# Optimization experiments

Measured on AMD Instinct MI355X. Metric: run time of the kernel, lower is better.

## Reference

```python
import jax, jax.numpy as jnp
import numpy as np

TEMPERATURE = 8.0  # sqrt(head_dim=64)
NEG_INF = -1e9


def setup_inputs() -> dict:
    key = jax.random.key(0)
    kq, kk, kv, km = jax.random.split(key, 4)
    B, H, S, D = 4, 16, 2048, 64
    q = jax.random.normal(kq, (B, H, S, D), dtype=jnp.float32)
    k = jax.random.normal(kk, (B, H, S, D), dtype=jnp.float32)
    v = jax.random.normal(kv, (B, H, S, D), dtype=jnp.float32)
    mask = jax.random.randint(km, (B, 1, S, S), 0, 2).astype(jnp.int32)
    return {"q": q, "k": k, "v": v, "mask": mask}


def reference(q, k, v, mask):
    # attn = (q / T) @ k^T  -> [B,H,S,S]
    attn = jnp.einsum('bhqd,bhkd->bhqk', q / TEMPERATURE, k)
    # masked_fill(mask == 0, -1e9)
    attn = jnp.where(mask == 0, NEG_INF, attn)
    # softmax over keys (dropout omitted: eval mode / deterministic baseline)
    attn = jax.nn.softmax(attn, axis=-1)
    out = jnp.einsum('bhqk,bhkd->bhqd', attn, v)
    return (out, attn)
```

## Files before the change

kernel.cpp:

```cpp
#include <hip/hip_runtime.h>
#include <stdint.h>

#define S_LEN 2048
#define DHEAD 64
#define BATCH 4
#define HEADS 16
#define QBLK 32
#define KBLK 64
#define NT 32
#define NBLK 4096
#define NEG_BIG (-1e9f)

typedef _Float16 half4v __attribute__((ext_vector_type(4)));
typedef _Float16 half8v __attribute__((ext_vector_type(8)));
typedef float floatx4 __attribute__((ext_vector_type(4)));

#define QH_OFF 0u
#define KH_OFF 16777216u
#define VT_OFF 33554432u
#define BM_OFF 50331648u

#define WAITV(N) asm volatile("s_waitcnt vmcnt(" #N ")" ::: "memory")
#define WAITL()  asm volatile("s_waitcnt lgkmcnt(0)" ::: "memory")
#define FENCE()  asm volatile("" ::: "memory")
#define BAR()    __builtin_amdgcn_s_barrier()

__device__ __forceinline__ void glds16(const void* g, void* l) {
    __builtin_amdgcn_global_load_lds(
        (const __attribute__((address_space(1))) uint32_t*)g,
        (__attribute__((address_space(3))) uint32_t*)(uint32_t)(uintptr_t)l,
        16, 0, 0);
}

__global__ __launch_bounds__(256) void prep_qk(const float* __restrict__ q, const float* __restrict__ k,
                                               _Float16* __restrict__ qh, _Float16* __restrict__ kh) {
    int i = blockIdx.x * 256 + threadIdx.x;
    const float* src; _Float16* dst; float s;
    if (i < 1048576) { src = q + (size_t)i * 8; dst = qh + (size_t)i * 8; s = 0.125f; }
    else { int j = i - 1048576; src = k + (size_t)j * 8; dst = kh + (size_t)j * 8; s = 1.0f; }
    floatx4 a = *(const floatx4*)src;
    floatx4 b = *(const floatx4*)(src + 4);
    half8v h;
    h[0]=(_Float16)(a[0]*s); h[1]=(_Float16)(a[1]*s); h[2]=(_Float16)(a[2]*s); h[3]=(_Float16)(a[3]*s);
    h[4]=(_Float16)(b[0]*s); h[5]=(_Float16)(b[1]*s); h[6]=(_Float16)(b[2]*s); h[7]=(_Float16)(b[3]*s);
    *(half8v*)dst = h;
}

__global__ __launch_bounds__(256) void prep_vt(const float* __restrict__ v, _Float16* __restrict__ vt) {
    __shared__ _Float16 lt[64][72];
    int bh = blockIdx.x >> 5;
    int s0 = (blockIdx.x & 31) * 64;
    int t  = threadIdx.x;
    {
        int row = t >> 2, dq = t & 3;
        const float* vb = v + ((size_t)bh * S_LEN + s0 + row) * DHEAD + dq * 16;
        #pragma unroll
        for (int q = 0; q < 4; ++q) {
            floatx4 val = *(const floatx4*)(vb + q * 4);
            #pragma unroll
            for (int j = 0; j < 4; ++j) lt[dq * 16 + q * 4 + j][row] = (_Float16)val[j];
        }
    }
    __syncthreads();
    {
        int d = t >> 2, kq = t & 3;
        half8v h0 = *(const half8v*)&lt[d][kq * 16];
        half8v h1 = *(const half8v*)&lt[d][kq * 16 + 8];
        _Float16* dst = vt + (size_t)bh * DHEAD * S_LEN + (size_t)d * S_LEN + s0 + kq * 16;
        *(half8v*)dst = h0;
        *(half8v*)(dst + 8) = h1;
    }
}

__global__ __launch_bounds__(256) void prep_bm(const int* __restrict__ mask, unsigned long long* __restrict__ bm) {
    int lane = threadIdx.x & 63, w = threadIdx.x >> 6;
    size_t row = (size_t)blockIdx.x * 4 + w;
    const int* mrow = mask + row * S_LEN;
    unsigned long long* brow = bm + row * 32;
    #pragma unroll 4
    for (int t = 0; t < 32; ++t) {
        unsigned long long bits = __ballot(mrow[t * 64 + lane] != 0);
        if (lane == 0) brow[t] = bits;
    }
}

__global__ __launch_bounds__(512, 8)
void attn_main(const _Float16* __restrict__ qh, const _Float16* __restrict__ kh,
               const _Float16* __restrict__ vt, const uint32_t* __restrict__ bm,
               float* __restrict__ outg, float* __restrict__ attng)
{
    __shared__ _Float16 kb[2][KBLK * DHEAD];
    __shared__ _Float16 vb[2][KBLK * DHEAD];
    __shared__ _Float16 pb[QBLK * KBLK];
    __shared__ float zb[4][QBLK];

    const int tid  = threadIdx.x;
    const int lane = tid & 63;
    const int w    = tid >> 6;
    const int c    = lane & 15;
    const int g    = lane >> 4;
    const int rh   = w >> 2;
    const int kgrp = w & 3;

    const int raw = blockIdx.x;
    const int lb  = (raw & 7) * (NBLK / 8) + (raw >> 3);
    const int bh  = lb >> 6;
    const int q0  = (lb & 63) * QBLK;
    const int bb  = bh >> 4;

    const _Float16* qp = qh + (size_t)bh * S_LEN * DHEAD;
    const char* kpc = (const char*)(kh + (size_t)bh * S_LEN * DHEAD);
    const char* vpc = (const char*)(vt + (size_t)bh * DHEAD * S_LEN);
    float* outp  = outg  + (size_t)bh * S_LEN * DHEAD;
    float* attnp = attng + (size_t)bh * S_LEN * S_LEN;

    const int srow = w * 8 + (lane >> 3);
    const int sq   = (lane & 7) ^ (srow & 7);
    const char* ksrc = kpc + srow * 128 + sq * 16;
    const char* vsrc = vpc + srow * (S_LEN * 2) + sq * 16;

    half8v qf0, qf1;
    {
        const _Float16* qb = qp + (q0 + rh * 16 + c) * DHEAD + g * 8;
        qf0 = *(const half8v*)qb;
        qf1 = *(const half8v*)(qb + 32);
    }

    const int keyl  = kgrp * 16 + c;
    const int koff0 = keyl * 128 + ((g ^ (c & 7)) << 4);
    const int koff1 = keyl * 128 + (((4 + g) ^ (c & 7)) << 4);
    const int prow  = rh * 16 + c;
    const int poff0 = prow * 128 + ((g ^ (c & 7)) << 4);
    const int poff1 = prow * 128 + (((4 + g) ^ (c & 7)) << 4);

    const int bmbit = (kgrp & 1) * 16 + c;
    const uint32_t* bmb = bm + ((size_t)bb * S_LEN + q0 + rh * 16 + g * 4) * (NT * 2) + (kgrp >> 1);

    int pwo0, pwo1, pwo2, pwo3;
    {
        int q8 = keyl >> 3, b2 = (keyl & 7) << 1;
        int r0 = rh * 16 + g * 4;
        pwo0 = (((r0 + 0) * 8 + (q8 ^ ((r0 + 0) & 7))) << 4) + b2;
        pwo1 = (((r0 + 1) * 8 + (q8 ^ ((r0 + 1) & 7))) << 4) + b2;
        pwo2 = (((r0 + 2) * 8 + (q8 ^ ((r0 + 2) & 7))) << 4) + b2;
        pwo3 = (((r0 + 3) * 8 + (q8 ^ ((r0 + 3) & 7))) << 4) + b2;
    }

    const int arow = tid >> 4, aq = tid & 15;
    const int aroff = ((arow * 8 + ((aq >> 1) ^ (arow & 7))) << 4) + ((aq & 1) << 3);
    float* abase = attnp + (size_t)(q0 + arow) * S_LEN + aq * 4;

    uint32_t bc0, bc1, bc2, bc3, bn0, bn1, bn2, bn3;

    float z0 = 0.f, z1 = 0.f, z2 = 0.f, z3 = 0.f;
    glds16(ksrc, (char*)&kb[0][0] + w * 1024);
    bc0 = bmb[0]; bc1 = bmb[64]; bc2 = bmb[128]; bc3 = bmb[192];
    #pragma unroll 1
    for (int t = 0; t < NT; ++t) {
        BAR(); FENCE();
        if (t + 1 < NT) {
            glds16(ksrc + (t + 1) * 8192, (char*)&kb[(t + 1) & 1][0] + w * 1024);
            int i2 = (t + 1) * 2;
            bn0 = bmb[i2]; bn1 = bmb[64 + i2]; bn2 = bmb[128 + i2]; bn3 = bmb[192 + i2];
            WAITV(5);
        } else { WAITV(0); }
        BAR(); FENCE();
        const char* kbB = (const char*)&kb[t & 1][0];
        half8v b0 = *(const half8v*)(kbB + koff0);
        half8v b1 = *(const half8v*)(kbB + koff1);
        floatx4 acc = {0.f, 0.f, 0.f, 0.f};
        acc = __builtin_amdgcn_mfma_f32_16x16x32_f16(qf0, b0, acc, 0, 0, 0);
        acc = __builtin_amdgcn_mfma_f32_16x16x32_f16(qf1, b1, acc, 0, 0, 0);
        z0 += __expf(((bc0 >> bmbit) & 1u) ? acc[0] : NEG_BIG);
        z1 += __expf(((bc1 >> bmbit) & 1u) ? acc[1] : NEG_BIG);
        z2 += __expf(((bc2 >> bmbit) & 1u) ? acc[2] : NEG_BIG);
        z3 += __expf(((bc3 >> bmbit) & 1u) ? acc[3] : NEG_BIG);
        bc0 = bn0; bc1 = bn1; bc2 = bn2; bc3 = bn3;
    }
    #pragma unroll
    for (int off = 1; off <= 8; off <<= 1) {
        z0 += __shfl_xor(z0, off); z1 += __shfl_xor(z1, off);
        z2 += __shfl_xor(z2, off); z3 += __shfl_xor(z3, off);
    }
    if (c == 0) {
        int r0 = rh * 16 + g * 4;
        zb[kgrp][r0] = z0; zb[kgrp][r0 + 1] = z1; zb[kgrp][r0 + 2] = z2; zb[kgrp][r0 + 3] = z3;
    }
    WAITL(); BAR(); FENCE();
    float r0_, r1_, r2_, r3_;
    {
        int r0 = rh * 16 + g * 4;
        r0_ = 1.f / (zb[0][r0] + zb[1][r0] + zb[2][r0] + zb[3][r0]);
        r1_ = 1.f / (zb[0][r0+1] + zb[1][r0+1] + zb[2][r0+1] + zb[3][r0+1]);
        r2_ = 1.f / (zb[0][r0+2] + zb[1][r0+2] + zb[2][r0+2] + zb[3][r0+2]);
        r3_ = 1.f / (zb[0][r0+3] + zb[1][r0+3] + zb[2][r0+3] + zb[3][r0+3]);
    }

    floatx4 o = {0.f, 0.f, 0.f, 0.f};
    glds16(ksrc, (char*)&kb[0][0] + w * 1024);
    glds16(vsrc, (char*)&vb[0][0] + w * 1024);
    bc0 = bmb[0]; bc1 = bmb[64]; bc2 = bmb[128]; bc3 = bmb[192];
    #pragma unroll 1
    for (int t = 0; t < NT; ++t) {
        BAR(); FENCE();
        if (t + 1 < NT) {
            glds16(ksrc + (t + 1) * 8192, (char*)&kb[(t + 1) & 1][0] + w * 1024);
            glds16(vsrc + (t + 1) * 128,  (char*)&vb[(t + 1) & 1][0] + w * 1024);
            int i2 = (t + 1) * 2;
            bn0 = bmb[i2]; bn1 = bmb[64 + i2]; bn2 = bmb[128 + i2]; bn3 = bmb[192 + i2];
            if (t == 0) { WAITV(6); } else { WAITV(7); }
        } else { WAITV(1); }
        BAR(); FENCE();
        const char* kbB = (const char*)&kb[t & 1][0];
        half8v b0 = *(const half8v*)(kbB + koff0);
        half8v b1 = *(const half8v*)(kbB + koff1);
        floatx4 acc = {0.f, 0.f, 0.f, 0.f};
        acc = __builtin_amdgcn_mfma_f32_16x16x32_f16(qf0, b0, acc, 0, 0, 0);
        acc = __builtin_amdgcn_mfma_f32_16x16x32_f16(qf1, b1, acc, 0, 0, 0);
        float p0 = __expf(((bc0 >> bmbit) & 1u) ? acc[0] : NEG_BIG) * r0_;
        float p1 = __expf(((bc1 >> bmbit) & 1u) ? acc[1] : NEG_BIG) * r1_;
        float p2 = __expf(((bc2 >> bmbit) & 1u) ? acc[2] : NEG_BIG) * r2_;
        float p3 = __expf(((bc3 >> bmbit) & 1u) ? acc[3] : NEG_BIG) * r3_;
        bc0 = bn0; bc1 = bn1; bc2 = bn2; bc3 = bn3;
        char* pbB = (char*)&pb[0];
        *(_Float16*)(pbB + pwo0) = (_Float16)p0;
        *(_Float16*)(pbB + pwo1) = (_Float16)p1;
        *(_Float16*)(pbB + pwo2) = (_Float16)p2;
        *(_Float16*)(pbB + pwo3) = (_Float16)p3;
        WAITL(); BAR(); FENCE();
        {
            half4v pv4 = *(const half4v*)((const char*)&pb[0] + aroff);
            floatx4 st = {(float)pv4[0], (float)pv4[1], (float)pv4[2], (float)pv4[3]};
            __builtin_nontemporal_store(st, (floatx4*)(abase + t * KBLK));
        }
        const char* vbB = (const char*)&vb[t & 1][0];
        half8v a0 = *(const half8v*)((const char*)&pb[0] + poff0);
        half8v a1 = *(const half8v*)((const char*)&pb[0] + poff1);
        half8v v0 = *(const half8v*)(vbB + koff0);
        half8v v1 = *(const half8v*)(vbB + koff1);
        o = __builtin_amdgcn_mfma_f32_16x16x32_f16(a0, v0, o, 0, 0, 0);
        o = __builtin_amdgcn_mfma_f32_16x16x32_f16(a1, v1, o, 0, 0, 0);
    }
    {
        float* ob = outp + (size_t)(q0 + rh * 16 + g * 4) * DHEAD + kgrp * 16 + c;
        ob[0] = o[0]; ob[DHEAD] = o[1]; ob[2 * DHEAD] = o[2]; ob[3 * DHEAD] = o[3];
    }
}

extern "C" void kernel_launch(void* const* d_in, const int* in_sizes, int n_in,
                              void* d_out, int out_size, void* d_ws, size_t ws_size,
                              hipStream_t stream) {
    const float* q    = (const float*)d_in[0];
    const float* k    = (const float*)d_in[1];
    const float* v    = (const float*)d_in[2];
    const int*   mask = (const int*)d_in[3];
    float* out  = (float*)d_out;
    float* attn = out + (size_t)BATCH * HEADS * S_LEN * DHEAD;

    char* ws = (char*)d_ws;
    _Float16* qhw = (_Float16*)(ws + QH_OFF);
    _Float16* khw = (_Float16*)(ws + KH_OFF);
    _Float16* vtw = (_Float16*)(ws + VT_OFF);
    unsigned long long* bmw = (unsigned long long*)(ws + BM_OFF);

    prep_qk<<<dim3(8192), dim3(256), 0, stream>>>(q, k, qhw, khw);
    prep_vt<<<dim3(2048), dim3(256), 0, stream>>>(v, vtw);
    prep_bm<<<dim3(2048), dim3(256), 0, stream>>>(mask, bmw);
    attn_main<<<dim3(NBLK), dim3(512), 0, stream>>>(qhw, khw, vtw, (const uint32_t*)bmw, out, attn);
}
```

Measured before the change: 376.7 us.

## Transpose QK^T MFMA to keep P in registers and split-K reduce PV

Measured after the change: 604.7 us. +60.5%, slower.

```diff
diff --git a/kernel.cpp b/kernel.cpp
--- a/kernel.cpp
+++ b/kernel.cpp
@@ -89,18 +89,18 @@
                const _Float16* __restrict__ vt, const uint32_t* __restrict__ bm,
                float* __restrict__ outg, float* __restrict__ attng)
 {
-    __shared__ _Float16 kb[2][KBLK * DHEAD];
-    __shared__ _Float16 vb[2][KBLK * DHEAD];
-    __shared__ _Float16 pb[QBLK * KBLK];
-    __shared__ float zb[4][QBLK];
+    __shared__ __attribute__((aligned(16))) char smem[33280];
+    char* kbuf = smem;
+    char* vbuf = smem + 16384;
+    float* zb  = (float*)(smem + 32768);
 
     const int tid  = threadIdx.x;
     const int lane = tid & 63;
     const int w    = tid >> 6;
     const int c    = lane & 15;
     const int g    = lane >> 4;
+    const int kg   = w & 3;
     const int rh   = w >> 2;
-    const int kgrp = w & 3;
 
     const int raw = blockIdx.x;
     const int lb  = (raw & 7) * (NBLK / 8) + (raw >> 3);
@@ -118,6 +118,8 @@
     const int sq   = (lane & 7) ^ (srow & 7);
     const char* ksrc = kpc + srow * 128 + sq * 16;
     const char* vsrc = vpc + srow * (S_LEN * 2) + sq * 16;
+    char* kdst = kbuf + w * 1024;
+    char* vdst = vbuf + w * 1024;
 
     half8v qf0, qf1;
     {
@@ -125,125 +127,109 @@
         qf0 = *(const half8v*)qb;
         qf1 = *(const half8v*)(qb + 32);
     }
-
-    const int keyl  = kgrp * 16 + c;
-    const int koff0 = keyl * 128 + ((g ^ (c & 7)) << 4);
-    const int koff1 = keyl * 128 + (((4 + g) ^ (c & 7)) << 4);
-    const int prow  = rh * 16 + c;
-    const int poff0 = prow * 128 + ((g ^ (c & 7)) << 4);
-    const int poff1 = prow * 128 + (((4 + g) ^ (c & 7)) << 4);
-
-    const int bmbit = (kgrp & 1) * 16 + c;
-    const uint32_t* bmb = bm + ((size_t)bb * S_LEN + q0 + rh * 16 + g * 4) * (NT * 2) + (kgrp >> 1);
-
-    int pwo0, pwo1, pwo2, pwo3;
-    {
-        int q8 = keyl >> 3, b2 = (keyl & 7) << 1;
-        int r0 = rh * 16 + g * 4;
-        pwo0 = (((r0 + 0) * 8 + (q8 ^ ((r0 + 0) & 7))) << 4) + b2;
-        pwo1 = (((r0 + 1) * 8 + (q8 ^ ((r0 + 1) & 7))) << 4) + b2;
-        pwo2 = (((r0 + 2) * 8 + (q8 ^ ((r0 + 2) & 7))) << 4) + b2;
-        pwo3 = (((r0 + 3) * 8 + (q8 ^ ((r0 + 3) & 7))) << 4) + b2;
-    }
-
-    const int arow = tid >> 4, aq = tid & 15;
-    const int aroff = ((arow * 8 + ((aq >> 1) ^ (arow & 7))) << 4) + ((aq & 1) << 3);
-    float* abase = attnp + (size_t)(q0 + arow) * S_LEN + aq * 4;
-
-    uint32_t bc0, bc1, bc2, bc3, bn0, bn1, bn2, bn3;
-
-    float z0 = 0.f, z1 = 0.f, z2 = 0.f, z3 = 0.f;
-    glds16(ksrc, (char*)&kb[0][0] + w * 1024);
-    bc0 = bmb[0]; bc1 = bmb[64]; bc2 = bmb[128]; bc3 = bmb[192];
+    const int koff0 = (kg * 16 + c) * 128 + ((g ^ (c & 7)) << 4);
+    const int koff1 = (kg * 16 + c) * 128 + (((4 + g) ^ (c & 7)) << 4);
+    const int voffb = c * 128 + ((((kg * 2) + (g >> 1)) ^ (c & 7)) << 4) + ((g & 1) << 3);
+    const int bmsh = (kg & 1) * 16 + g * 4;
+    const uint32_t* bmb = bm + ((size_t)bb * S_LEN + q0 + rh * 16 + c) * 64 + (kg >> 1);
+
+    float z = 0.f;
+    glds16(ksrc, kdst);
+    FENCE();
+    uint32_t bc = bmb[0], bn = 0;
     #pragma unroll 1
     for (int t = 0; t < NT; ++t) {
+        FENCE();
+        WAITV(1);
         BAR(); FENCE();
         if (t + 1 < NT) {
-            glds16(ksrc + (t + 1) * 8192, (char*)&kb[(t + 1) & 1][0] + w * 1024);
-            int i2 = (t + 1) * 2;
-            bn0 = bmb[i2]; bn1 = bmb[64 + i2]; bn2 = bmb[128 + i2]; bn3 = bmb[192 + i2];
-            WAITV(5);
-        } else { WAITV(0); }
-        BAR(); FENCE();
-        const char* kbB = (const char*)&kb[t & 1][0];
-        half8v b0 = *(const half8v*)(kbB + koff0);
-        half8v b1 = *(const half8v*)(kbB + koff1);
+            glds16(ksrc + (t + 1) * 8192, kdst + (((t + 1) & 1) << 13));
+            FENCE();
+            bn = bmb[(t + 1) * 2];
+        }
+        const char* kbB = kbuf + ((t & 1) << 13);
+        half8v kf0 = *(const half8v*)(kbB + koff0);
+        half8v kf1 = *(const half8v*)(kbB + koff1);
         floatx4 acc = {0.f, 0.f, 0.f, 0.f};
-        acc = __builtin_amdgcn_mfma_f32_16x16x32_f16(qf0, b0, acc, 0, 0, 0);
-        acc = __builtin_amdgcn_mfma_f32_16x16x32_f16(qf1, b1, acc, 0, 0, 0);
-        z0 += __expf(((bc0 >> bmbit) & 1u) ? acc[0] : NEG_BIG);
-        z1 += __expf(((bc1 >> bmbit) & 1u) ? acc[1] : NEG_BIG);
-        z2 += __expf(((bc2 >> bmbit) & 1u) ? acc[2] : NEG_BIG);
-        z3 += __expf(((bc3 >> bmbit) & 1u) ? acc[3] : NEG_BIG);
-        bc0 = bn0; bc1 = bn1; bc2 = bn2; bc3 = bn3;
-    }
-    #pragma unroll
-    for (int off = 1; off <= 8; off <<= 1) {
-        z0 += __shfl_xor(z0, off); z1 += __shfl_xor(z1, off);
-        z2 += __shfl_xor(z2, off); z3 += __shfl_xor(z3, off);
-    }
-    if (c == 0) {
-        int r0 = rh * 16 + g * 4;
-        zb[kgrp][r0] = z0; zb[kgrp][r0 + 1] = z1; zb[kgrp][r0 + 2] = z2; zb[kgrp][r0 + 3] = z3;
-    }
+        acc = __builtin_amdgcn_mfma_f32_16x16x32_f16(kf0, qf0, acc, 0, 0, 0);
+        acc = __builtin_amdgcn_mfma_f32_16x16x32_f16(kf1, qf1, acc, 0, 0, 0);
+        unsigned bits = bc >> bmsh;
+        z += __expf((bits & 1u) ? acc[0] : NEG_BIG) + __expf((bits & 2u) ? acc[1] : NEG_BIG)
+           + __expf((bits & 4u) ? acc[2] : NEG_BIG) + __expf((bits & 8u) ? acc[3] : NEG_BIG);
+        bc = bn;
+    }
+    z += __shfl_xor(z, 16);
+    z += __shfl_xor(z, 32);
+    if (g == 0) zb[kg * 32 + rh * 16 + c] = z;
     WAITL(); BAR(); FENCE();
-    float r0_, r1_, r2_, r3_;
-    {
-        int r0 = rh * 16 + g * 4;
-        r0_ = 1.f / (zb[0][r0] + zb[1][r0] + zb[2][r0] + zb[3][r0]);
-        r1_ = 1.f / (zb[0][r0+1] + zb[1][r0+1] + zb[2][r0+1] + zb[3][r0+1]);
-        r2_ = 1.f / (zb[0][r0+2] + zb[1][r0+2] + zb[2][r0+2] + zb[3][r0+2]);
-        r3_ = 1.f / (zb[0][r0+3] + zb[1][r0+3] + zb[2][r0+3] + zb[3][r0+3]);
-    }
-
-    floatx4 o = {0.f, 0.f, 0.f, 0.f};
-    glds16(ksrc, (char*)&kb[0][0] + w * 1024);
-    glds16(vsrc, (char*)&vb[0][0] + w * 1024);
-    bc0 = bmb[0]; bc1 = bmb[64]; bc2 = bmb[128]; bc3 = bmb[192];
+    const int row = rh * 16 + c;
+    const float r = 1.0f / (zb[row] + zb[32 + row] + zb[64 + row] + zb[96 + row]);
+
+    floatx4 o0 = {0.f,0.f,0.f,0.f}, o1 = o0, o2 = o0, o3 = o0;
+    float* abase = attnp + (size_t)(q0 + rh * 16 + c) * S_LEN + kg * 16 + g * 4;
+    glds16(ksrc, kdst);
+    glds16(vsrc, vdst);
+    FENCE();
+    bc = bmb[0];
     #pragma unroll 1
     for (int t = 0; t < NT; ++t) {
+        FENCE();
+        if (t == 0) { WAITV(1); } else { WAITV(2); }
         BAR(); FENCE();
         if (t + 1 < NT) {
-            glds16(ksrc + (t + 1) * 8192, (char*)&kb[(t + 1) & 1][0] + w * 1024);
-            glds16(vsrc + (t + 1) * 128,  (char*)&vb[(t + 1) & 1][0] + w * 1024);
-            int i2 = (t + 1) * 2;
-            bn0 = bmb[i2]; bn1 = bmb[64 + i2]; bn2 = bmb[128 + i2]; bn3 = bmb[192 + i2];
-            if (t == 0) { WAITV(6); } else { WAITV(7); }
-        } else { WAITV(1); }
-        BAR(); FENCE();
-        const char* kbB = (const char*)&kb[t & 1][0];
-        half8v b0 = *(const half8v*)(kbB + koff0);
-        half8v b1 = *(const half8v*)(kbB + koff1);
+            glds16(ksrc + (t + 1) * 8192, kdst + (((t + 1) & 1) << 13));
+            glds16(vsrc + (t + 1) * 128,  vdst + (((t + 1) & 1) << 13));
+            FENCE();
+            bn = bmb[(t + 1) * 2];
+        }
+        const char* kbB = kbuf + ((t & 1) << 13);
+        const char* vbB = vbuf + ((t & 1) << 13);
+        half8v kf0 = *(const half8v*)(kbB + koff0);
+        half8v kf1 = *(const half8v*)(kbB + koff1);
         floatx4 acc = {0.f, 0.f, 0.f, 0.f};
-        acc = __builtin_amdgcn_mfma_f32_16x16x32_f16(qf0, b0, acc, 0, 0, 0);
-        acc = __builtin_amdgcn_mfma_f32_16x16x32_f16(qf1, b1, acc, 0, 0, 0);
-        float p0 = __expf(((bc0 >> bmbit) & 1u) ? acc[0] : NEG_BIG) * r0_;
-        float p1 = __expf(((bc1 >> bmbit) & 1u) ? acc[1] : NEG_BIG) * r1_;
-        float p2 = __expf(((bc2 >> bmbit) & 1u) ? acc[2] : NEG_BIG) * r2_;
-        float p3 = __expf(((bc3 >> bmbit) & 1u) ? acc[3] : NEG_BIG) * r3_;
-        bc0 = bn0; bc1 = bn1; bc2 = bn2; bc3 = bn3;
-        char* pbB = (char*)&pb[0];
-        *(_Float16*)(pbB + pwo0) = (_Float16)p0;
-        *(_Float16*)(pbB + pwo1) = (_Float16)p1;
-        *(_Float16*)(pbB + pwo2) = (_Float16)p2;
-        *(_Float16*)(pbB + pwo3) = (_Float16)p3;
-        WAITL(); BAR(); FENCE();
-        {
-            half4v pv4 = *(const half4v*)((const char*)&pb[0] + aroff);
-            floatx4 st = {(float)pv4[0], (float)pv4[1], (float)pv4[2], (float)pv4[3]};
-            __builtin_nontemporal_store(st, (floatx4*)(abase + t * KBLK));
-        }
-        const char* vbB = (const char*)&vb[t & 1][0];
-        half8v a0 = *(const half8v*)((const char*)&pb[0] + poff0);
-        half8v a1 = *(const half8v*)((const char*)&pb[0] + poff1);
-        half8v v0 = *(const half8v*)(vbB + koff0);
-        half8v v1 = *(const half8v*)(vbB + koff1);
-        o = __builtin_amdgcn_mfma_f32_16x16x32_f16(a0, v0, o, 0, 0, 0);
-        o = __builtin_amdgcn_mfma_f32_16x16x32_f16(a1, v1, o, 0, 0, 0);
-    }
-    {
-        float* ob = outp + (size_t)(q0 + rh * 16 + g * 4) * DHEAD + kgrp * 16 + c;
-        ob[0] = o[0]; ob[DHEAD] = o[1]; ob[2 * DHEAD] = o[2]; ob[3 * DHEAD] = o[3];
+        acc = __builtin_amdgcn_mfma_f32_16x16x32_f16(kf0, qf0, acc, 0, 0, 0);
+        acc = __builtin_amdgcn_mfma_f32_16x16x32_f16(kf1, qf1, acc, 0, 0, 0);
+        unsigned bits = bc >> bmsh;
+        float p0 = __expf((bits & 1u) ? acc[0] : NEG_BIG) * r;
+        float p1 = __expf((bits & 2u) ? acc[1] : NEG_BIG) * r;
+        float p2 = __expf((bits & 4u) ? acc[2] : NEG_BIG) * r;
+        float p3 = __expf((bits & 8u) ? acc[3] : NEG_BIG) * r;
+        bc = bn;
+        floatx4 st = {p0, p1, p2, p3};
+        *(floatx4*)(abase + t * KBLK) = st;
+        half4v af; af[0] = (_Float16)p0; af[1] = (_Float16)p1;
+        af[2] = (_Float16)p2; af[3] = (_Float16)p3;
+        half4v bv0 = *(const half4v*)(vbB + voffb);
+        half4v bv1 = *(const half4v*)(vbB + voffb + 2048);
+        half4v bv2 = *(const half4v*)(vbB + voffb + 4096);
+        half4v bv3 = *(const half4v*)(vbB + voffb + 6144);
+        o0 = __builtin_amdgcn_mfma_f32_16x16x16f16(af, bv0, o0, 0, 0, 0);
+        o1 = __builtin_amdgcn_mfma_f32_16x16x16f16(af, bv1, o1, 0, 0, 0);
+        o2 = __builtin_amdgcn_mfma_f32_16x16x16f16(af, bv2, o2, 0, 0, 0);
+        o3 = __builtin_amdgcn_mfma_f32_16x16x16f16(af, bv3, o3, 0, 0, 0);
+    }
+
+    FENCE(); WAITL(); BAR(); FENCE();
+    floatx4* rbuf = (floatx4*)smem;
+    if (kg != 0) {
+        floatx4* rb = rbuf + ((kg - 1) * 2 + rh) * 256 + lane;
+        rb[0] = o0; rb[64] = o1; rb[128] = o2; rb[192] = o3;
+    }
+    WAITL(); BAR(); FENCE();
+    if (kg == 0) {
+        const int s0 = rh * 256 + lane;
+        o0 += rbuf[s0]       + rbuf[512 + s0]       + rbuf[1024 + s0];
+        o1 += rbuf[s0 + 64]  + rbuf[512 + s0 + 64]  + rbuf[1024 + s0 + 64];
+        o2 += rbuf[s0 + 128] + rbuf[512 + s0 + 128] + rbuf[1024 + s0 + 128];
+        o3 += rbuf[s0 + 192] + rbuf[512 + s0 + 192] + rbuf[1024 + s0 + 192];
+        float* ob = outp + (size_t)(q0 + rh * 16 + g * 4) * DHEAD + c;
+        #pragma unroll
+        for (int i = 0; i < 4; ++i) {
+            ob[i * DHEAD]      = o0[i];
+            ob[i * DHEAD + 16] = o1[i];
+            ob[i * DHEAD + 32] = o2[i];
+            ob[i * DHEAD + 48] = o3[i];
+        }
     }
 }
 
```

## Make first softmax pass barrier-free with per-wave private K buffers

Applied to the files above, without the earlier changes.

Result: no change. 380.9 us (+1.1%).

```diff
diff --git a/kernel.cpp b/kernel.cpp
--- a/kernel.cpp
+++ b/kernel.cpp
@@ -89,18 +89,19 @@
                const _Float16* __restrict__ vt, const uint32_t* __restrict__ bm,
                float* __restrict__ outg, float* __restrict__ attng)
 {
-    __shared__ _Float16 kb[2][KBLK * DHEAD];
-    __shared__ _Float16 vb[2][KBLK * DHEAD];
-    __shared__ _Float16 pb[QBLK * KBLK];
-    __shared__ float zb[4][QBLK];
+    __shared__ __attribute__((aligned(16))) char smem[37376];
+    char* kbuf = smem;
+    char* vbuf = smem + 16384;
+    char* pb   = smem + 32768;
+    float* zbf = (float*)(smem + 36864);
 
     const int tid  = threadIdx.x;
     const int lane = tid & 63;
     const int w    = tid >> 6;
     const int c    = lane & 15;
     const int g    = lane >> 4;
+    const int kg   = w & 3;
     const int rh   = w >> 2;
-    const int kgrp = w & 3;
 
     const int raw = blockIdx.x;
     const int lb  = (raw & 7) * (NBLK / 8) + (raw >> 3);
@@ -114,10 +115,12 @@
     float* outp  = outg  + (size_t)bh * S_LEN * DHEAD;
     float* attnp = attng + (size_t)bh * S_LEN * S_LEN;
 
-    const int srow = w * 8 + (lane >> 3);
+    const int srow = tid >> 3;
     const int sq   = (lane & 7) ^ (srow & 7);
     const char* ksrc = kpc + srow * 128 + sq * 16;
     const char* vsrc = vpc + srow * (S_LEN * 2) + sq * 16;
+    char* kdst = kbuf + w * 1024;
+    char* vdst = vbuf + w * 1024;
 
     half8v qf0, qf1;
     {
@@ -125,19 +128,20 @@
         qf0 = *(const half8v*)qb;
         qf1 = *(const half8v*)(qb + 32);
     }
-
-    const int keyl  = kgrp * 16 + c;
-    const int koff0 = keyl * 128 + ((g ^ (c & 7)) << 4);
-    const int koff1 = keyl * 128 + (((4 + g) ^ (c & 7)) << 4);
+    const int koff0 = (kg * 16 + c) * 128 + ((g ^ (c & 7)) << 4);
+    const int koff1 = (kg * 16 + c) * 128 + (((4 + g) ^ (c & 7)) << 4);
     const int prow  = rh * 16 + c;
     const int poff0 = prow * 128 + ((g ^ (c & 7)) << 4);
     const int poff1 = prow * 128 + (((4 + g) ^ (c & 7)) << 4);
-
-    const int bmbit = (kgrp & 1) * 16 + c;
-    const uint32_t* bmb = bm + ((size_t)bb * S_LEN + q0 + rh * 16 + g * 4) * (NT * 2) + (kgrp >> 1);
+    const int koff0p = c * 128 + ((g ^ (c & 7)) << 4);
+    const int koff1p = c * 128 + (((4 + g) ^ (c & 7)) << 4);
+
+    const int bmbit = (kg & 1) * 16 + c;
+    const uint32_t* bmb = bm + ((size_t)bb * S_LEN + q0 + rh * 16 + g * 4) * 64 + (kg >> 1);
 
     int pwo0, pwo1, pwo2, pwo3;
     {
+        int keyl = kg * 16 + c;
         int q8 = keyl >> 3, b2 = (keyl & 7) << 1;
         int r0 = rh * 16 + g * 4;
         pwo0 = (((r0 + 0) * 8 + (q8 ^ ((r0 + 0) & 7))) << 4) + b2;
@@ -145,73 +149,90 @@
         pwo2 = (((r0 + 2) * 8 + (q8 ^ ((r0 + 2) & 7))) << 4) + b2;
         pwo3 = (((r0 + 3) * 8 + (q8 ^ ((r0 + 3) & 7))) << 4) + b2;
     }
-
-    const int arow = tid >> 4, aq = tid & 15;
-    const int aroff = ((arow * 8 + ((aq >> 1) ^ (arow & 7))) << 4) + ((aq & 1) << 3);
-    float* abase = attnp + (size_t)(q0 + arow) * S_LEN + aq * 4;
-
-    uint32_t bc0, bc1, bc2, bc3, bn0, bn1, bn2, bn3;
+    const int ar = tid >> 4, aq = tid & 15;
+    const int proff = ar * 128 + (((aq >> 1) ^ (ar & 7)) << 4) + ((aq & 1) << 3);
+    float* abase = attnp + (size_t)(q0 + ar) * S_LEN + aq * 4;
 
     float z0 = 0.f, z1 = 0.f, z2 = 0.f, z3 = 0.f;
-    glds16(ksrc, (char*)&kb[0][0] + w * 1024);
+    char* myb = smem + w * 4096;
+    const char* kps = kpc + kg * 2048 + (lane >> 3) * 128
+                    + (((lane & 7) ^ ((lane >> 3) & 7)) << 4);
+    glds16(kps, myb);
+    glds16(kps + 1024, myb + 1024);
+    FENCE();
+    uint32_t bc0 = bmb[0], bc1 = bmb[64], bc2 = bmb[128], bc3 = bmb[192];
+    FENCE();
+    glds16(kps + 8192, myb + 2048);
+    glds16(kps + 9216, myb + 3072);
+    FENCE();
+    uint32_t bn0 = 0, bn1 = 0, bn2 = 0, bn3 = 0;
+    #pragma unroll 1
+    for (int t = 0; t < NT; ++t) {
+        FENCE();
+        if (t == NT - 1) { WAITV(0); } else { WAITV(2); }
+        char* kbB = myb + ((t & 1) << 11);
+        half8v kf0 = *(const half8v*)(kbB + koff0p);
+        half8v kf1 = *(const half8v*)(kbB + koff1p);
+        WAITL(); FENCE();
+        if (t + 1 < NT) {
+            int i2 = (t + 1) * 2;
+            bn0 = bmb[i2]; bn1 = bmb[64 + i2]; bn2 = bmb[128 + i2]; bn3 = bmb[192 + i2];
+            FENCE();
+        }
+        if (t + 2 < NT) {
+            const char* s = kps + (t + 2) * 8192;
+            glds16(s, kbB);
+            glds16(s + 1024, kbB + 1024);
+            FENCE();
+        }
+        floatx4 acc = {0.f, 0.f, 0.f, 0.f};
+        acc = __builtin_amdgcn_mfma_f32_16x16x32_f16(qf0, kf0, acc, 0, 0, 0);
+        acc = __builtin_amdgcn_mfma_f32_16x16x32_f16(qf1, kf1, acc, 0, 0, 0);
+        z0 += __expf(((bc0 >> bmbit) & 1u) ? acc[0] : NEG_BIG);
+        z1 += __expf(((bc1 >> bmbit) & 1u) ? acc[1] : NEG_BIG);
+        z2 += __expf(((bc2 >> bmbit) & 1u) ? acc[2] : NEG_BIG);
+        z3 += __expf(((bc3 >> bmbit) & 1u) ? acc[3] : NEG_BIG);
+        bc0 = bn0; bc1 = bn1; bc2 = bn2; bc3 = bn3;
+    }
+    #pragma unroll
+    for (int off = 1; off <= 8; off <<= 1) {
+        z0 += __shfl_xor(z0, off); z1 += __shfl_xor(z1, off);
+        z2 += __shfl_xor(z2, off); z3 += __shfl_xor(z3, off);
+    }
+    if (c == 0) {
+        int r0 = rh * 16 + g * 4;
+        zbf[kg * 32 + r0] = z0; zbf[kg * 32 + r0 + 1] = z1;
+        zbf[kg * 32 + r0 + 2] = z2; zbf[kg * 32 + r0 + 3] = z3;
+    }
+    WAITL(); BAR(); FENCE();
+    float r0_, r1_, r2_, r3_;
+    {
+        int r0 = rh * 16 + g * 4;
+        r0_ = 1.f / (zbf[r0] + zbf[32 + r0] + zbf[64 + r0] + zbf[96 + r0]);
+        r1_ = 1.f / (zbf[r0+1] + zbf[32 + r0+1] + zbf[64 + r0+1] + zbf[96 + r0+1]);
+        r2_ = 1.f / (zbf[r0+2] + zbf[32 + r0+2] + zbf[64 + r0+2] + zbf[96 + r0+2]);
+        r3_ = 1.f / (zbf[r0+3] + zbf[32 + r0+3] + zbf[64 + r0+3] + zbf[96 + r0+3]);
+    }
+    BAR(); FENCE();
+
+    floatx4 o = {0.f, 0.f, 0.f, 0.f};
+    glds16(ksrc, kdst);
+    glds16(vsrc, vdst);
+    FENCE();
     bc0 = bmb[0]; bc1 = bmb[64]; bc2 = bmb[128]; bc3 = bmb[192];
     #pragma unroll 1
     for (int t = 0; t < NT; ++t) {
         BAR(); FENCE();
         if (t + 1 < NT) {
-            glds16(ksrc + (t + 1) * 8192, (char*)&kb[(t + 1) & 1][0] + w * 1024);
-            int i2 = (t + 1) * 2;
-            bn0 = bmb[i2]; bn1 = bmb[64 + i2]; bn2 = bmb[128 + i2]; bn3 = bmb[192 + i2];
-            WAITV(5);
-        } else { WAITV(0); }
-        BAR(); FENCE();
-        const char* kbB = (const char*)&kb[t & 1][0];
-        half8v b0 = *(const half8v*)(kbB + koff0);
-        half8v b1 = *(const half8v*)(kbB + koff1);
-        floatx4 acc = {0.f, 0.f, 0.f, 0.f};
-        acc = __builtin_amdgcn_mfma_f32_16x16x32_f16(qf0, b0, acc, 0, 0, 0);
-        acc = __builtin_amdgcn_mfma_f32_16x16x32_f16(qf1, b1, acc, 0, 0, 0);
-        z0 += __expf(((bc0 >> bmbit) & 1u) ? acc[0] : NEG_BIG);
-        z1 += __expf(((bc1 >> bmbit) & 1u) ? acc[1] : NEG_BIG);
-        z2 += __expf(((bc2 >> bmbit) & 1u) ? acc[2] : NEG_BIG);
-        z3 += __expf(((bc3 >> bmbit) & 1u) ? acc[3] : NEG_BIG);
-        bc0 = bn0; bc1 = bn1; bc2 = bn2; bc3 = bn3;
-    }
-    #pragma unroll
-    for (int off = 1; off <= 8; off <<= 1) {
-        z0 += __shfl_xor(z0, off); z1 += __shfl_xor(z1, off);
-        z2 += __shfl_xor(z2, off); z3 += __shfl_xor(z3, off);
-    }
-    if (c == 0) {
-        int r0 = rh * 16 + g * 4;
-        zb[kgrp][r0] = z0; zb[kgrp][r0 + 1] = z1; zb[kgrp][r0 + 2] = z2; zb[kgrp][r0 + 3] = z3;
-    }
-    WAITL(); BAR(); FENCE();
-    float r0_, r1_, r2_, r3_;
-    {
-        int r0 = rh * 16 + g * 4;
-        r0_ = 1.f / (zb[0][r0] + zb[1][r0] + zb[2][r0] + zb[3][r0]);
-        r1_ = 1.f / (zb[0][r0+1] + zb[1][r0+1] + zb[2][r0+1] + zb[3][r0+1]);
-        r2_ = 1.f / (zb[0][r0+2] + zb[1][r0+2] + zb[2][r0+2] + zb[3][r0+2]);
-        r3_ = 1.f / (zb[0][r0+3] + zb[1][r0+3] + zb[2][r0+3] + zb[3][r0+3]);
-    }
-
-    floatx4 o = {0.f, 0.f, 0.f, 0.f};
-    glds16(ksrc, (char*)&kb[0][0] + w * 1024);
-    glds16(vsrc, (char*)&vb[0][0] + w * 1024);
-    bc0 = bmb[0]; bc1 = bmb[64]; bc2 = bmb[128]; bc3 = bmb[192];
-    #pragma unroll 1
-    for (int t = 0; t < NT; ++t) {
-        BAR(); FENCE();
-        if (t + 1 < NT) {
-            glds16(ksrc + (t + 1) * 8192, (char*)&kb[(t + 1) & 1][0] + w * 1024);
-            glds16(vsrc + (t + 1) * 128,  (char*)&vb[(t + 1) & 1][0] + w * 1024);
+            glds16(ksrc + (t + 1) * 8192, kdst + (((t + 1) & 1) << 13));
+            glds16(vsrc + (t + 1) * 128,  vdst + (((t + 1) & 1) << 13));
             int i2 = (t + 1) * 2;
             bn0 = bmb[i2]; bn1 = bmb[64 + i2]; bn2 = bmb[128 + i2]; bn3 = bmb[192 + i2];
             if (t == 0) { WAITV(6); } else { WAITV(7); }
         } else { WAITV(1); }
         BAR(); FENCE();
-        const char* kbB = (const char*)&kb[t & 1][0];
+        const char* kbB = kbuf + ((t & 1) << 13);
+        const char* vbB = vbuf + ((t & 1) << 13);
         half8v b0 = *(const half8v*)(kbB + koff0);
         half8v b1 = *(const half8v*)(kbB + koff1);
         floatx4 acc = {0.f, 0.f, 0.f, 0.f};
@@ -222,27 +243,25 @@
         float p2 = __expf(((bc2 >> bmbit) & 1u) ? acc[2] : NEG_BIG) * r2_;
         float p3 = __expf(((bc3 >> bmbit) & 1u) ? acc[3] : NEG_BIG) * r3_;
         bc0 = bn0; bc1 = bn1; bc2 = bn2; bc3 = bn3;
-        char* pbB = (char*)&pb[0];
-        *(_Float16*)(pbB + pwo0) = (_Float16)p0;
-        *(_Float16*)(pbB + pwo1) = (_Float16)p1;
-        *(_Float16*)(pbB + pwo2) = (_Float16)p2;
-        *(_Float16*)(pbB + pwo3) = (_Float16)p3;
+        *(_Float16*)(pb + pwo0) = (_Float16)p0;
+        *(_Float16*)(pb + pwo1) = (_Float16)p1;
+        *(_Float16*)(pb + pwo2) = (_Float16)p2;
+        *(_Float16*)(pb + pwo3) = (_Float16)p3;
         WAITL(); BAR(); FENCE();
         {
-            half4v pv4 = *(const half4v*)((const char*)&pb[0] + aroff);
+            half4v pv4 = *(const half4v*)(pb + proff);
             floatx4 st = {(float)pv4[0], (float)pv4[1], (float)pv4[2], (float)pv4[3]};
             __builtin_nontemporal_store(st, (floatx4*)(abase + t * KBLK));
         }
-        const char* vbB = (const char*)&vb[t & 1][0];
-        half8v a0 = *(const half8v*)((const char*)&pb[0] + poff0);
-        half8v a1 = *(const half8v*)((const char*)&pb[0] + poff1);
+        half8v a0 = *(const half8v*)(pb + poff0);
+        half8v a1 = *(const half8v*)(pb + poff1);
         half8v v0 = *(const half8v*)(vbB + koff0);
         half8v v1 = *(const half8v*)(vbB + koff1);
         o = __builtin_amdgcn_mfma_f32_16x16x32_f16(a0, v0, o, 0, 0, 0);
         o = __builtin_amdgcn_mfma_f32_16x16x32_f16(a1, v1, o, 0, 0, 0);
     }
     {
-        float* ob = outp + (size_t)(q0 + rh * 16 + g * 4) * DHEAD + kgrp * 16 + c;
+        float* ob = outp + (size_t)(q0 + rh * 16 + g * 4) * DHEAD + kg * 16 + c;
         ob[0] = o[0]; ob[DHEAD] = o[1]; ob[2 * DHEAD] = o[2]; ob[3 * DHEAD] = o[3];
     }
 }
```

## Single-pass QK with register-cached exp values and unnormalized PV accumulation

Applied to the files above, without the earlier changes.

After: 413.2 us. +9.7%, slower.

```diff
diff --git a/kernel.cpp b/kernel.cpp
--- a/kernel.cpp
+++ b/kernel.cpp
@@ -5,10 +5,10 @@
 #define DHEAD 64
 #define BATCH 4
 #define HEADS 16
-#define QBLK 32
-#define KBLK 64
-#define NT 32
-#define NBLK 4096
+#define QBLK 16
+#define KBLK 128
+#define NT 16
+#define NBLK 8192
 #define NEG_BIG (-1e9f)
 
 typedef _Float16 half4v __attribute__((ext_vector_type(4)));
@@ -84,28 +84,29 @@
     }
 }
 
-__global__ __launch_bounds__(512, 8)
+__global__ __launch_bounds__(512, 4)
 void attn_main(const _Float16* __restrict__ qh, const _Float16* __restrict__ kh,
                const _Float16* __restrict__ vt, const uint32_t* __restrict__ bm,
                float* __restrict__ outg, float* __restrict__ attng)
 {
-    __shared__ _Float16 kb[2][KBLK * DHEAD];
-    __shared__ _Float16 vb[2][KBLK * DHEAD];
-    __shared__ _Float16 pb[QBLK * KBLK];
-    __shared__ float zb[4][QBLK];
+    __shared__ __attribute__((aligned(16))) char smem[70144];
+    char* kbuf = smem;
+    char* vbuf = smem + 32768;
+    char* pb   = smem + 65536;
+    float* zbf = (float*)(smem + 69632);
 
     const int tid  = threadIdx.x;
     const int lane = tid & 63;
     const int w    = tid >> 6;
     const int c    = lane & 15;
     const int g    = lane >> 4;
-    const int rh   = w >> 2;
-    const int kgrp = w & 3;
+    const int kc2  = w & 3;
+    const int dc   = w >> 2;
 
     const int raw = blockIdx.x;
     const int lb  = (raw & 7) * (NBLK / 8) + (raw >> 3);
-    const int bh  = lb >> 6;
-    const int q0  = (lb & 63) * QBLK;
+    const int bh  = lb >> 7;
+    const int q0  = (lb & 127) * QBLK;
     const int bb  = bh >> 4;
 
     const _Float16* qp = qh + (size_t)bh * S_LEN * DHEAD;
@@ -114,136 +115,161 @@
     float* outp  = outg  + (size_t)bh * S_LEN * DHEAD;
     float* attnp = attng + (size_t)bh * S_LEN * S_LEN;
 
-    const int srow = w * 8 + (lane >> 3);
-    const int sq   = (lane & 7) ^ (srow & 7);
-    const char* ksrc = kpc + srow * 128 + sq * 16;
-    const char* vsrc = vpc + srow * (S_LEN * 2) + sq * 16;
+    const int ksrow = tid >> 3;
+    const char* ksrcA = kpc + ksrow * 128 + (((tid & 7) ^ (ksrow & 7)) << 4);
+    const int vsd = tid >> 4;
+    const int vswz = ((tid & 15) ^ (vsd & 15)) << 4;
+    const char* vsrcA = vpc + vsd * 4096 + vswz;
+    const char* vsrcB = vpc + (32 + vsd) * 4096 + vswz;
 
     half8v qf0, qf1;
     {
-        const _Float16* qb = qp + (q0 + rh * 16 + c) * DHEAD + g * 8;
+        const _Float16* qb = qp + (size_t)(q0 + c) * DHEAD + g * 8;
         qf0 = *(const half8v*)qb;
         qf1 = *(const half8v*)(qb + 32);
     }
 
-    const int keyl  = kgrp * 16 + c;
-    const int koff0 = keyl * 128 + ((g ^ (c & 7)) << 4);
-    const int koff1 = keyl * 128 + (((4 + g) ^ (c & 7)) << 4);
-    const int prow  = rh * 16 + c;
-    const int poff0 = prow * 128 + ((g ^ (c & 7)) << 4);
-    const int poff1 = prow * 128 + (((4 + g) ^ (c & 7)) << 4);
-
-    const int bmbit = (kgrp & 1) * 16 + c;
-    const uint32_t* bmb = bm + ((size_t)bb * S_LEN + q0 + rh * 16 + g * 4) * (NT * 2) + (kgrp >> 1);
-
+    const int kk = w * 16 + c;
+    const int koff0 = kk * 128 + ((g ^ (kk & 7)) << 4);
+    const int koff1 = kk * 128 + (((4 + g) ^ (kk & 7)) << 4);
+
+    const int vd0 = dc * 32 + c, vd1 = vd0 + 16;
+    const int voff0 = vd0 * 256 + (((kc2 * 4 + g) ^ (vd0 & 15)) << 4);
+    const int voff1 = vd1 * 256 + (((kc2 * 4 + g) ^ (vd1 & 15)) << 4);
+
+    const int q8 = kk >> 3;
     int pwo0, pwo1, pwo2, pwo3;
     {
-        int q8 = keyl >> 3, b2 = (keyl & 7) << 1;
-        int r0 = rh * 16 + g * 4;
-        pwo0 = (((r0 + 0) * 8 + (q8 ^ ((r0 + 0) & 7))) << 4) + b2;
-        pwo1 = (((r0 + 1) * 8 + (q8 ^ ((r0 + 1) & 7))) << 4) + b2;
-        pwo2 = (((r0 + 2) * 8 + (q8 ^ ((r0 + 2) & 7))) << 4) + b2;
-        pwo3 = (((r0 + 3) * 8 + (q8 ^ ((r0 + 3) & 7))) << 4) + b2;
-    }
-
-    const int arow = tid >> 4, aq = tid & 15;
-    const int aroff = ((arow * 8 + ((aq >> 1) ^ (arow & 7))) << 4) + ((aq & 1) << 3);
-    float* abase = attnp + (size_t)(q0 + arow) * S_LEN + aq * 4;
-
+        int r0 = g * 4;
+        pwo0 = (r0 + 0) * 256 + (((q8 ^ (r0 + 0)) & 15) << 4) + (kk & 7) * 2;
+        pwo1 = (r0 + 1) * 256 + (((q8 ^ (r0 + 1)) & 15) << 4) + (kk & 7) * 2;
+        pwo2 = (r0 + 2) * 256 + (((q8 ^ (r0 + 2)) & 15) << 4) + (kk & 7) * 2;
+        pwo3 = (r0 + 3) * 256 + (((q8 ^ (r0 + 3)) & 15) << 4) + (kk & 7) * 2;
+    }
+    const int poff = c * 256 + (((kc2 * 4 + g) ^ c) << 4);
+    const int srr  = tid >> 5, sk4 = tid & 31;
+    const int proff = srr * 256 + ((((sk4 >> 1) ^ srr) & 15) << 4) + (sk4 & 1) * 8;
+    float* abase = attnp + (size_t)(q0 + srr) * S_LEN + sk4 * 4;
+
+    const uint32_t* bmb = bm + ((size_t)bb * S_LEN + q0 + g * 4) * 64 + (w >> 1);
+    const int bmsh = (w & 1) * 16 + c;
+
+    half4v p[NT];
+    float z0 = 0.f, z1 = 0.f, z2 = 0.f, z3 = 0.f;
+    floatx4 o0 = {0.f, 0.f, 0.f, 0.f}, o1 = o0;
     uint32_t bc0, bc1, bc2, bc3, bn0, bn1, bn2, bn3;
 
-    float z0 = 0.f, z1 = 0.f, z2 = 0.f, z3 = 0.f;
-    glds16(ksrc, (char*)&kb[0][0] + w * 1024);
-    bc0 = bmb[0]; bc1 = bmb[64]; bc2 = bmb[128]; bc3 = bmb[192];
-    #pragma unroll 1
+    {
+        char* kd = kbuf + tid * 16;
+        char* vd = vbuf + tid * 16;
+        glds16(ksrcA, kd); glds16(ksrcA + 8192, kd + 8192);
+        glds16(vsrcA, vd); glds16(vsrcB, vd + 8192);
+        FENCE();
+        bc0 = bmb[0]; bc1 = bmb[64]; bc2 = bmb[128]; bc3 = bmb[192];
+        FENCE();
+    }
+    #pragma unroll
     for (int t = 0; t < NT; ++t) {
         BAR(); FENCE();
         if (t + 1 < NT) {
-            glds16(ksrc + (t + 1) * 8192, (char*)&kb[(t + 1) & 1][0] + w * 1024);
-            int i2 = (t + 1) * 2;
-            bn0 = bmb[i2]; bn1 = bmb[64 + i2]; bn2 = bmb[128 + i2]; bn3 = bmb[192 + i2];
-            WAITV(5);
+            const char* s = ksrcA + (t + 1) * 16384;
+            char* kd = kbuf + (((t + 1) & 1) << 14) + tid * 16;
+            glds16(s, kd); glds16(s + 8192, kd + 8192);
+            char* vd = vbuf + (((t + 1) & 1) << 14) + tid * 16;
+            glds16(vsrcA + (t + 1) * 256, vd);
+            glds16(vsrcB + (t + 1) * 256, vd + 8192);
+            FENCE();
+            int i4 = (t + 1) * 4;
+            bn0 = bmb[i4]; bn1 = bmb[64 + i4]; bn2 = bmb[128 + i4]; bn3 = bmb[192 + i4];
+            WAITV(8);
         } else { WAITV(0); }
         BAR(); FENCE();
-        const char* kbB = (const char*)&kb[t & 1][0];
-        half8v b0 = *(const half8v*)(kbB + koff0);
-        half8v b1 = *(const half8v*)(kbB + koff1);
+        const char* kbB = kbuf + ((t & 1) << 14);
+        const char* vbB = vbuf + ((t & 1) << 14);
+        half8v kf0 = *(const half8v*)(kbB + koff0);
+        half8v kf1 = *(const half8v*)(kbB + koff1);
         floatx4 acc = {0.f, 0.f, 0.f, 0.f};
-        acc = __builtin_amdgcn_mfma_f32_16x16x32_f16(qf0, b0, acc, 0, 0, 0);
-        acc = __builtin_amdgcn_mfma_f32_16x16x32_f16(qf1, b1, acc, 0, 0, 0);
-        z0 += __expf(((bc0 >> bmbit) & 1u) ? acc[0] : NEG_BIG);
-        z1 += __expf(((bc1 >> bmbit) & 1u) ? acc[1] : NEG_BIG);
-        z2 += __expf(((bc2 >> bmbit) & 1u) ? acc[2] : NEG_BIG);
-        z3 += __expf(((bc3 >> bmbit) & 1u) ? acc[3] : NEG_BIG);
+        acc = __builtin_amdgcn_mfma_f32_16x16x32_f16(qf0, kf0, acc, 0, 0, 0);
+        acc = __builtin_amdgcn_mfma_f32_16x16x32_f16(qf1, kf1, acc, 0, 0, 0);
+        float e0 = __expf(((bc0 >> bmsh) & 1u) ? acc[0] : NEG_BIG);
+        float e1 = __expf(((bc1 >> bmsh) & 1u) ? acc[1] : NEG_BIG);
+        float e2 = __expf(((bc2 >> bmsh) & 1u) ? acc[2] : NEG_BIG);
+        float e3 = __expf(((bc3 >> bmsh) & 1u) ? acc[3] : NEG_BIG);
+        z0 += e0; z1 += e1; z2 += e2; z3 += e3;
         bc0 = bn0; bc1 = bn1; bc2 = bn2; bc3 = bn3;
-    }
+        half4v ph; ph[0] = (_Float16)e0; ph[1] = (_Float16)e1;
+        ph[2] = (_Float16)e2; ph[3] = (_Float16)e3;
+        p[t] = ph;
+        *(_Float16*)(pb + pwo0) = ph[0];
+        *(_Float16*)(pb + pwo1) = ph[1];
+        *(_Float16*)(pb + pwo2) = ph[2];
+        *(_Float16*)(pb + pwo3) = ph[3];
+        WAITL(); BAR(); FENCE();
+        half8v af  = *(const half8v*)(pb + poff);
+        half8v vf0 = *(const half8v*)(vbB + voff0);
+        half8v vf1 = *(const half8v*)(vbB + voff1);
+        o0 = __builtin_amdgcn_mfma_f32_16x16x32_f16(af, vf0, o0, 0, 0, 0);
+        o1 = __builtin_amdgcn_mfma_f32_16x16x32_f16(af, vf1, o1, 0, 0, 0);
+    }
+
     #pragma unroll
     for (int off = 1; off <= 8; off <<= 1) {
         z0 += __shfl_xor(z0, off); z1 += __shfl_xor(z1, off);
         z2 += __shfl_xor(z2, off); z3 += __shfl_xor(z3, off);
     }
     if (c == 0) {
-        int r0 = rh * 16 + g * 4;
-        zb[kgrp][r0] = z0; zb[kgrp][r0 + 1] = z1; zb[kgrp][r0 + 2] = z2; zb[kgrp][r0 + 3] = z3;
+        zbf[w * 16 + g * 4 + 0] = z0; zbf[w * 16 + g * 4 + 1] = z1;
+        zbf[w * 16 + g * 4 + 2] = z2; zbf[w * 16 + g * 4 + 3] = z3;
     }
     WAITL(); BAR(); FENCE();
     float r0_, r1_, r2_, r3_;
     {
-        int r0 = rh * 16 + g * 4;
-        r0_ = 1.f / (zb[0][r0] + zb[1][r0] + zb[2][r0] + zb[3][r0]);
-        r1_ = 1.f / (zb[0][r0+1] + zb[1][r0+1] + zb[2][r0+1] + zb[3][r0+1]);
-        r2_ = 1.f / (zb[0][r0+2] + zb[1][r0+2] + zb[2][r0+2] + zb[3][r0+2]);
-        r3_ = 1.f / (zb[0][r0+3] + zb[1][r0+3] + zb[2][r0+3] + zb[3][r0+3]);
-    }
-
-    floatx4 o = {0.f, 0.f, 0.f, 0.f};
-    glds16(ksrc, (char*)&kb[0][0] + w * 1024);
-    glds16(vsrc, (char*)&vb[0][0] + w * 1024);
-    bc0 = bmb[0]; bc1 = bmb[64]; bc2 = bmb[128]; bc3 = bmb[192];
-    #pragma unroll 1
+        float s0 = 0.f, s1 = 0.f, s2 = 0.f, s3 = 0.f;
+        #pragma unroll
+        for (int ww = 0; ww < 8; ++ww) {
+            s0 += zbf[ww * 16 + g * 4 + 0]; s1 += zbf[ww * 16 + g * 4 + 1];
+            s2 += zbf[ww * 16 + g * 4 + 2]; s3 += zbf[ww * 16 + g * 4 + 3];
+        }
+        r0_ = 1.f / s0; r1_ = 1.f / s1; r2_ = 1.f / s2; r3_ = 1.f / s3;
+    }
+    o0[0] *= r0_; o0[1] *= r1_; o0[2] *= r2_; o0[3] *= r3_;
+    o1[0] *= r0_; o1[1] *= r1_; o1[2] *= r2_; o1[3] *= r3_;
+
+    #pragma unroll
     for (int t = 0; t < NT; ++t) {
         BAR(); FENCE();
-        if (t + 1 < NT) {
-            glds16(ksrc + (t + 1) * 8192, (char*)&kb[(t + 1) & 1][0] + w * 1024);
-            glds16(vsrc + (t + 1) * 128,  (char*)&vb[(t + 1) & 1][0] + w * 1024);
-            int i2 = (t + 1) * 2;
-            bn0 = bmb[i2]; bn1 = bmb[64 + i2]; bn2 = bmb[128 + i2]; bn3 = bmb[192 + i2];
-            if (t == 0) { WAITV(6); } else { WAITV(7); }
-        } else { WAITV(1); }
-        BAR(); FENCE();
-        const char* kbB = (const char*)&kb[t & 1][0];
-        half8v b0 = *(const half8v*)(kbB + koff0);
-        half8v b1 = *(const half8v*)(kbB + koff1);
-        floatx4 acc = {0.f, 0.f, 0.f, 0.f};
-        acc = __builtin_amdgcn_mfma_f32_16x16x32_f16(qf0, b0, acc, 0, 0, 0);
-        acc = __builtin_amdgcn_mfma_f32_16x16x32_f16(qf1, b1, acc, 0, 0, 0);
-        float p0 = __expf(((bc0 >> bmbit) & 1u) ? acc[0] : NEG_BIG) * r0_;
-        float p1 = __expf(((bc1 >> bmbit) & 1u) ? acc[1] : NEG_BIG) * r1_;
-        float p2 = __expf(((bc2 >> bmbit) & 1u) ? acc[2] : NEG_BIG) * r2_;
-        float p3 = __expf(((bc3 >> bmbit) & 1u) ? acc[3] : NEG_BIG) * r3_;
-        bc0 = bn0; bc1 = bn1; bc2 = bn2; bc3 = bn3;
-        char* pbB = (char*)&pb[0];
-        *(_Float16*)(pbB + pwo0) = (_Float16)p0;
-        *(_Float16*)(pbB + pwo1) = (_Float16)p1;
-        *(_Float16*)(pbB + pwo2) = (_Float16)p2;
-        *(_Float16*)(pbB + pwo3) = (_Float16)p3;
+        half4v ph = p[t];
+        *(_Float16*)(pb + pwo0) = (_Float16)((float)ph[0] * r0_);
+        *(_Float16*)(pb + pwo1) = (_Float16)((float)ph[1] * r1_);
+        *(_Float16*)(pb + pwo2) = (_Float16)((float)ph[2] * r2_);
+        *(_Float16*)(pb + pwo3) = (_Float16)((float)ph[3] * r3_);
         WAITL(); BAR(); FENCE();
-        {
-            half4v pv4 = *(const half4v*)((const char*)&pb[0] + aroff);
-            floatx4 st = {(float)pv4[0], (float)pv4[1], (float)pv4[2], (float)pv4[3]};
-            __builtin_nontemporal_store(st, (floatx4*)(abase + t * KBLK));
+        half4v pv4 = *(const half4v*)(pb + proff);
+        floatx4 st = {(float)pv4[0], (float)pv4[1], (float)pv4[2], (float)pv4[3]};
+        __builtin_nontemporal_store(st, (floatx4*)(abase + t * KBLK));
+    }
+
+    BAR(); FENCE();
+    float* rbuf = (float*)smem;
+    {
+        int base = w * 528 + (g * 4) * 33 + c;
+        rbuf[base]           = o0[0]; rbuf[base + 33]      = o0[1];
+        rbuf[base + 66]      = o0[2]; rbuf[base + 99]      = o0[3];
+        rbuf[base + 16]      = o1[0]; rbuf[base + 33 + 16] = o1[1];
+        rbuf[base + 66 + 16] = o1[2]; rbuf[base + 99 + 16] = o1[3];
+    }
+    WAITL(); BAR(); FENCE();
+    {
+        int r_ = tid >> 5, d2 = (tid & 31) * 2;
+        int dcc = d2 >> 5;
+        float v0 = 0.f, v1 = 0.f;
+        #pragma unroll
+        for (int k2 = 0; k2 < 4; ++k2) {
+            int base = (dcc * 4 + k2) * 528 + r_ * 33 + (d2 & 31);
+            v0 += rbuf[base]; v1 += rbuf[base + 1];
         }
-        const char* vbB = (const char*)&vb[t & 1][0];
-        half8v a0 = *(const half8v*)((const char*)&pb[0] + poff0);
-        half8v a1 = *(const half8v*)((const char*)&pb[0] + poff1);
-        half8v v0 = *(const half8v*)(vbB + koff0);
-        half8v v1 = *(const half8v*)(vbB + koff1);
-        o = __builtin_amdgcn_mfma_f32_16x16x32_f16(a0, v0, o, 0, 0, 0);
-        o = __builtin_amdgcn_mfma_f32_16x16x32_f16(a1, v1, o, 0, 0, 0);
-    }
-    {
-        float* ob = outp + (size_t)(q0 + rh * 16 + g * 4) * DHEAD + kgrp * 16 + c;
-        ob[0] = o[0]; ob[DHEAD] = o[1]; ob[2 * DHEAD] = o[2]; ob[3 * DHEAD] = o[3];
+        float2 st = make_float2(v0, v1);
+        *(float2*)(outp + (size_t)(q0 + r_) * DHEAD + d2) = st;
     }
 }
 
```
